# Performance work log

Hardware: AMD Instinct MI355X
Metric: run time of the kernel (lower is better)

The kernel has to match this reference:

```python
import jax, jax.numpy as jnp
from jax import lax
import numpy as np

SR = 44100
PI = 3.14159  # matches the constant used in the torch source
FREQ_HZ = 100.0
FREQ_RAD = 2.0 * PI * FREQ_HZ / SR
N_SAMPLES = 4_410_000  # 100 s of audio; exactly 10000 wavetable chunks of 441


def biquad_lowpass(x, f, q):
    # torchaudio.functional.lowpass_biquad, direct form II transposed
    w0 = 2.0 * jnp.pi * f / SR
    cosw = jnp.cos(w0)
    alpha = jnp.sin(w0) / (2.0 * q)
    b0 = (1.0 - cosw) / 2.0
    b1 = 1.0 - cosw
    b2 = (1.0 - cosw) / 2.0
    a0 = 1.0 + alpha
    a1 = -2.0 * cosw
    a2 = 1.0 - alpha
    b0, b1, b2, a1, a2 = b0 / a0, b1 / a0, b2 / a0, a1 / a0, a2 / a0

    def step(carry, xn):
        s1, s2 = carry
        y = b0 * xn + s1
        s1n = b1 * xn - a1 * y + s2
        s2n = b2 * xn - a2 * y
        return (s1n, s2n), y

    zero = jnp.zeros((), x.dtype)
    _, y = lax.scan(step, (zero, zero), x)
    return y


def setup_inputs() -> dict:
    key = jax.random.key(0)
    ks = jax.random.split(key, 6)
    wsz = int(SR // FREQ_HZ)  # 441
    return {
        "feedback_line": 0.1 * jax.random.normal(ks[0], (N_SAMPLES,), jnp.float32),
        "h": jax.random.uniform(ks[1], (1, 9), jnp.float32),
        "t": jnp.arange(N_SAMPLES, dtype=jnp.float32) / SR,
        "wavetable_noise": 2.0 * jax.random.uniform(ks[2], (wsz,), jnp.float32) - 1.0,
        "W1": 0.1 * jax.random.normal(ks[3], (9, 128), jnp.float32),
        "b1": jnp.zeros((128,), jnp.float32),
        "W2": 0.1 * jax.random.normal(ks[4], (128, 5), jnp.float32),
        "b2": jnp.array([0.5, 1.0, 0.5, 0.05, 1.0], jnp.float32),
        "lp_cutoff": jnp.float32(8000.0),  # LearnableLowpass(sr, 8000.0)
        "env_params": jnp.array([0.1, 1.0, 0.5], jnp.float32),  # LearnableASR(3): attack, sustain, release
        "fade": jnp.linspace(1.0, 0.0, 256, dtype=jnp.float32),
        "freq_rad": FREQ_RAD,  # static python float
        "output_length_samples": N_SAMPLES,  # static python int
    }


def reference(feedback_line, h, t, wavetable_noise, W1, b1, W2, b2, lp_cutoff, env_params, fade, freq_rad, output_length_samples):
    # hamps_to_decay MLP: Linear(9,128) -> ReLU -> Linear(128,5) -> ReLU
    latents = jax.nn.relu(jax.nn.relu(h @ W1 + b1) @ W2 + b2)  # [1, 5]
    decay = jnp.clip(latents[0, 0] / 10.0 + 0.9, 0.9, 0.999)

    freq = freq_rad * SR / (2.0 * PI)
    wsz = int(SR // freq)  # static wavetable size

    # wavetable = 2*rand-1, then biquad lowpass with learned cutoff/Q, then LearnableLowpass
    lowpass_freq = jnp.clip(latents[0, 1] * SR / 4.0, 100.0, SR / 2.0 - 1.0)
    lowpass_q = jnp.clip(latents[0, 2], 0.1, 0.999)
    wt = biquad_lowpass(wavetable_noise, lowpass_freq, lowpass_q)
    wt = biquad_lowpass(wt, lp_cutoff, jnp.float32(0.707))  # self.lowpass

    feedbackamt = latents[0, 3]
    wt = lax.stop_gradient(wt)  # original detaches the wavetable before the recurrence

    # Karplus-Strong recurrence over chunks: sequential scan (data-dependent across steps)
    n_chunks = output_length_samples // wsz
    fb = feedback_line[: n_chunks * wsz].reshape(n_chunks, wsz)

    def step(cur, fb_chunk):
        cur = cur + feedbackamt * fb_chunk
        cur = decay * 0.5 * (cur + jnp.roll(cur, 1))
        return cur, cur

    last, chunks = lax.scan(step, wt, fb)
    samples = chunks.reshape(-1)

    rem = output_length_samples % wsz
    if rem > 0:  # static python branch
        extra = decay * 0.5 * (last + jnp.roll(last, 1))
        samples = jnp.concatenate([samples, extra[:rem]])

    out = samples.at[-256:].multiply(fade)

    # LearnableASR envelope: attack ramp, sustain level, release ramp
    a = jnp.abs(env_params[0]) + 1e-3
    s = env_params[1]
    r = jnp.abs(env_params[2]) + 1e-3
    T = t[-1]
    env = jnp.clip(t / a, 0.0, 1.0) * jnp.clip((T - t) / r, 0.0, 1.0) * s

    return out * env * latents[0, 4]
```

## Files before the change

kernel.cpp:

```cpp
#include <hip/hip_runtime.h>
#include <utility>

#define N_SAMP   4410000
#define WSZ      441
#define NC       10000
#define NB       250
#define LB       40
#define HB       20
#define TILEF    (LB*WSZ)
#define RD       16
#define TWO_PI_F 6.28318530717958647692f
#define FADE_START (N_SAMP - 256)
#define INV_SR   (1.0f/44100.0f)
#define INV441   (1.0f/441.0f)

#define WS_WT   0
#define WS_SLOT(a) (448 + (a)*448)
#define WS_NEED ((size_t)(448 + (NB-1)*448) * sizeof(float))

static_assert(NB * LB == NC, "block decomposition");
static_assert(LB == 2*HB, "two flush phases");

template <class F, int... Is>
__device__ __forceinline__ void unroll_impl(F f, std::integer_sequence<int, Is...>) {
    (f(std::integral_constant<int, Is>{}), ...);
}
template <int N, class F>
__device__ __forceinline__ void unroll_for(F f) {
    unroll_impl(f, std::make_integer_sequence<int, N>{});
}

__device__ __forceinline__ float hwsin(float rev) { return __builtin_amdgcn_sinf(rev); }
__device__ __forceinline__ float hwcos(float rev) { return __builtin_amdgcn_cosf(rev); }

__device__ __forceinline__ void gl2lds16(const float* gsrc_lane, float* lds_base_uniform) {
    __builtin_amdgcn_global_load_lds(
        (const __attribute__((address_space(1))) void*)gsrc_lane,
        (__attribute__((address_space(3))) void*)lds_base_uniform,
        16, 0, 0);
}

__device__ __forceinline__ void stage_tile7(const float* __restrict__ g,
                                            float* __restrict__ l,
                                            int nfloats, int tid) {
    const int wave = tid >> 6, lane = tid & 63;
    const int nfull = nfloats >> 8;
    for (int c = wave; c < nfull; c += 7)
        gl2lds16(g + (c << 8) + lane*4, l + (c << 8));
    const int rem = nfloats & 255;
    if (rem && wave == 0 && lane*4 < rem) {
        const int base = nfull << 8;
        gl2lds16(g + base + lane*4, l + base);
    }
}

__device__ __forceinline__ void bq_coefs(float f, float q,
    float& b0, float& b1, float& b2, float& a1, float& a2)
{
    float w0 = TWO_PI_F * f / 44100.0f;
    float cw = cosf(w0), sw = sinf(w0);
    float al = sw / (2.0f * q);
    float a0 = 1.0f + al;
    b0 = ((1.0f - cw) * 0.5f) / a0;
    b1 = (1.0f - cw) / a0;
    b2 = ((1.0f - cw) * 0.5f) / a0;
    a1 = (-2.0f * cw) / a0;
    a2 = (1.0f - al) / a0;
}

__device__ __forceinline__ void run_biquads(const float* __restrict__ noise,
    float lpf, float lpq, float f2, float* dst)
{
    float c10,c11,c12,c13,c14, c20,c21,c22,c23,c24;
    bq_coefs(lpf, lpq, c10,c11,c12,c13,c14);
    bq_coefs(f2, 0.707f, c20,c21,c22,c23,c24);
    float s11=0.f,s12=0.f,s21=0.f,s22=0.f;
    for (int m = 0; m < WSZ; ++m) {
        float x  = noise[m];
        float y1 = c10*x + s11;
        s11 = c11*x - c13*y1 + s12;
        s12 = c12*x - c14*y1;
        float y2 = c20*y1 + s21;
        s21 = c21*y1 - c23*y2 + s22;
        s22 = c22*y1 - c24*y2;
        dst[m] = y2;
    }
}

__device__ __forceinline__ void mlp_latents(
    const float* __restrict__ h, const float* __restrict__ W1,
    const float* __restrict__ b1v, const float* __restrict__ W2,
    const float* __restrict__ b2v, int lane, float lat[5])
{
    float hc0 = b1v[lane], hc1 = b1v[lane + 64];
    #pragma unroll
    for (int i = 0; i < 9; ++i) {
        float hv = h[i];
        hc0 = fmaf(hv, W1[i*128 + lane], hc0);
        hc1 = fmaf(hv, W1[i*128 + lane + 64], hc1);
    }
    hc0 = fmaxf(hc0, 0.f); hc1 = fmaxf(hc1, 0.f);
    float part[5];
    #pragma unroll
    for (int m = 0; m < 5; ++m)
        part[m] = fmaf(hc0, W2[lane*5 + m], hc1 * W2[(lane+64)*5 + m]);
    #pragma unroll
    for (int off = 32; off > 0; off >>= 1) {
        #pragma unroll
        for (int m = 0; m < 5; ++m)
            part[m] += __shfl_xor(part[m], off);
    }
    #pragma unroll
    for (int m = 0; m < 5; ++m)
        lat[m] = fmaxf(part[m] + b2v[m], 0.f);
}

__device__ __forceinline__ void biquad_wave(const float xin[7], float yout[7],
    float f, float q, int l)
{
    float b0,b1,b2,a1,a2;
    bq_coefs(f, q, b0,b1,b2,a1,a2);
    const float t1c = b1 - a1*b0;
    const float t2c = b2 - a2*b0;
    float m00=1.f,m01=0.f,m10=0.f,m11=1.f;
    float cv0=0.f, cv1=0.f;
    #pragma unroll
    for (int k = 0; k < 7; ++k) {
        float x = xin[k];
        float n0 = -a1*cv0 + cv1 + t1c*x;
        float n1 = -a2*cv0 + t2c*x;
        cv0 = n0; cv1 = n1;
        float r00 = -a1*m00 + m10, r01 = -a1*m01 + m11;
        float r10 = -a2*m00,       r11 = -a2*m01;
        m00=r00; m01=r01; m10=r10; m11=r11;
    }
    #pragma unroll
    for (int d = 1; d < 64; d <<= 1) {
        int srcl = l - d; int s2 = srcl < 0 ? 0 : srcl;
        float pm00=__shfl(m00,s2), pm01=__shfl(m01,s2);
        float pm10=__shfl(m10,s2), pm11=__shfl(m11,s2);
        float pc0=__shfl(cv0,s2), pc1=__shfl(cv1,s2);
        if (srcl >= 0) {
            float nc0 = m00*pc0 + m01*pc1 + cv0;
            float nc1 = m10*pc0 + m11*pc1 + cv1;
            float n00 = m00*pm00 + m01*pm10;
            float n01 = m00*pm01 + m01*pm11;
            float n10 = m10*pm00 + m11*pm10;
            float n11 = m10*pm01 + m11*pm11;
            m00=n00; m01=n01; m10=n10; m11=n11; cv0=nc0; cv1=nc1;
        }
    }
    int esrc = (l == 0) ? 0 : l - 1;
    float e0 = __shfl(cv0, esrc);
    float e1 = __shfl(cv1, esrc);
    float s1  = (l == 0) ? 0.f : e0;
    float s2v = (l == 0) ? 0.f : e1;
    #pragma unroll
    for (int k = 0; k < 7; ++k) {
        float x = xin[k];
        float y = b0*x + s1;
        float ns1 = b1*x - a1*y + s2v;
        s2v = b2*x - a2*y;
        s1 = ns1;
        yout[k] = y;
    }
}

__device__ __forceinline__ void fft441_fwd(const float* v, float* Zr, float* Zi,
    const float* c441, const float* s441, float* ws_slot, int tid)
{
    if (tid < 441) {
        const int bq = tid / 21, c = tid - 21*bq;
        float yr = 0.f, yi = 0.f;
        int pm = 0;
        #pragma unroll
        for (int a = 0; a < 21; ++a) {
            float x = v[21*a + bq];
            float cc = c441[21*pm], ss = s441[21*pm];
            yr = fmaf(x,  cc, yr);
            yi = fmaf(-x, ss, yi);
            pm += c; if (pm >= 21) pm -= 21;
        }
        const int bc = bq * c;
        float cB = c441[bc], sB = s441[bc];
        Zr[c*21 + bq] = yr*cB + yi*sB;
        Zi[c*21 + bq] = yi*cB - yr*sB;
    }
    __syncthreads();
    if (tid < 441) {
        const int c = tid / 21, d = tid - 21*c;
        float xr = 0.f, xi = 0.f;
        int pm = 0;
        const float* zr = Zr + c*21;
        const float* zi = Zi + c*21;
        #pragma unroll
        for (int bq = 0; bq < 21; ++bq) {
            float cc = c441[21*pm], ss = s441[21*pm];
            float gr = zr[bq], gi = zi[bq];
            xr = fmaf(gr, cc, fmaf(gi,  ss, xr));
            xi = fmaf(gi, cc, fmaf(-gr, ss, xi));
            pm += d; if (pm >= 21) pm -= 21;
        }
        const int jm = c + 21*d;
        if (jm < 221) {
            ws_slot[jm]       = xr;
            ws_slot[224 + jm] = xi;
        }
    }
}

__device__ __forceinline__ void fft441_inv(const float* SrF, const float* SiF,
    float* Hr, float* Hi, const float* c441, const float* s441,
    float* e_lds, int tid)
{
    if (tid < 441) {
        const int bq = tid / 21, c = tid - 21*bq;
        float gr = 0.f, gi = 0.f;
        int pm = 0;
        #pragma unroll
        for (int a = 0; a < 21; ++a) {
            float sr = SrF[21*a + bq], si = SiF[21*a + bq];
            float cc = c441[21*pm], ss = s441[21*pm];
            gr = fmaf(sr, cc, fmaf(-si, ss, gr));
            gi = fmaf(sr, ss, fmaf( si, cc, gi));
            pm += c; if (pm >= 21) pm -= 21;
        }
        const int bc = bq * c;
        float cB = c441[bc], sB = s441[bc];
        Hr[c*21 + bq] = gr*cB - gi*sB;
        Hi[c*21 + bq] = gr*sB + gi*cB;
    }
    __syncthreads();
    if (tid < 441) {
        const int c = tid / 21, d = tid - 21*c;
        float acc = 0.f;
        int pm = 0;
        const float* hr = Hr + c*21;
        const float* hi = Hi + c*21;
        #pragma unroll
        for (int bq = 0; bq < 21; ++bq) {
            float cc = c441[21*pm], ss = s441[21*pm];
            acc = fmaf(hr[bq], cc, fmaf(-hi[bq], ss, acc));
            pm += d; if (pm >= 21) pm -= 21;
        }
        e_lds[c + 21*d] = acc * (1.0f/441.0f);
    }
}

__global__ __launch_bounds__(448, 1) void k_front(
    const float* __restrict__ fb, const float* __restrict__ h,
    const float* __restrict__ noise, const float* __restrict__ W1,
    const float* __restrict__ b1v, const float* __restrict__ W2,
    const float* __restrict__ b2v, const float* __restrict__ lpcut,
    float* __restrict__ ws)
{
    __shared__ __align__(16) float fbL[TILEF + 24];
    __shared__ __align__(16) float v_lds[448];
    __shared__ __align__(16) float Zr[441], Zi[441];
    __shared__ float c441[441], s441[441];
    const int b = blockIdx.x;
    const int tid = threadIdx.x;
    const bool w0 = tid < 64;
    const int j = tid;
    const bool act = w0 && (j < 63);
    const int i0 = b * LB;

    stage_tile7(fb + i0*WSZ, fbL, TILEF, tid);
    if (tid < 441) {
        float ph = (float)tid * INV441;
        c441[tid] = hwcos(ph);
        s441[tid] = hwsin(ph);
    }

    float lat[5];
    mlp_latents(h, W1, b1v, W2, b2v, tid & 63, lat);
    const float decay = fminf(fmaxf(lat[0]/10.0f + 0.9f, 0.9f), 0.999f);
    const float famt  = lat[3];
    const float d2 = 0.5f * decay;
    const int src = (j == 0) ? 62 : j - 1;

    float cur[7];
    #pragma unroll
    for (int k = 0; k < 7; ++k) cur[k] = 0.f;
    if (w0 && b == 0) {
        const float lpf = fminf(fmaxf(lat[1]*44100.0f/4.0f, 100.0f), 22049.0f);
        const float lpq = fminf(fmaxf(lat[2], 0.1f), 0.999f);
        const float f2  = lpcut[0];
        float xin[7], y1[7], y2[7];
        #pragma unroll
        for (int k = 0; k < 7; ++k) xin[k] = act ? noise[7*j + k] : 0.f;
        biquad_wave(xin, y1, lpf, lpq, j);
        biquad_wave(y1, y2, f2, 0.707f, j);
        #pragma unroll
        for (int k = 0; k < 7; ++k) {
            cur[k] = act ? y2[k] : 0.f;
            if (act) ws[WS_WT + 7*j + k] = y2[k];
        }
    }
    __syncthreads();

    if (w0) {
        unroll_for<LB>([&](auto I) {
            constexpr int i = decltype(I)::value;
            float x[7];
            #pragma unroll
            for (int k = 0; k < 7; ++k) {
                float fv = act ? fbL[i*WSZ + 7*j + k] : 0.f;
                x[k] = fmaf(famt, fv, cur[k]);
            }
            float x6p = __shfl(x[6], src);
            cur[0] = d2 * (x[0] + x6p);
            #pragma unroll
            for (int k = 1; k < 7; ++k)
                cur[k] = d2 * (x[k] + x[k-1]);
        });
        if (act) {
            #pragma unroll
            for (int k = 0; k < 7; ++k) v_lds[7*j + k] = cur[k];
        }
    }
    __syncthreads();

    fft441_fwd(v_lds, Zr, Zi, c441, s441, ws + WS_SLOT(b), tid);
}

__global__ __launch_bounds__(256, 1) void k_scan(
    const float* __restrict__ h, const float* __restrict__ W1,
    const float* __restrict__ b1v, const float* __restrict__ W2,
    const float* __restrict__ b2v, float* __restrict__ ws)
{
    const int tid = threadIdx.x;
    float lat[5];
    mlp_latents(h, W1, b1v, W2, b2v, tid & 63, lat);
    const float decay = fminf(fmaxf(lat[0]/10.0f + 0.9f, 0.9f), 0.999f);
    if (tid >= 221) return;
    const float s = hwsin((float)tid * INV441);
    const float c = hwcos((float)tid * INV441);
    float lr = 0.5f*decay*(1.0f + c);
    float li = -0.5f*decay*s;
    float pr = 1.0f, pi = 0.0f, br = lr, bi = li;
    int e = LB;
    while (e) {
        if (e & 1) { float t = pr*br - pi*bi; pi = pr*bi + pi*br; pr = t; }
        float t2 = br*br - bi*bi; bi = 2.0f*br*bi; br = t2;
        e >>= 1;
    }
    const int NV = NB - 1;
    float sr = 0.0f, si = 0.0f;
    float cr[RD], ci[RD];
    #pragma unroll
    for (int d = 0; d < RD; ++d) {
        int idx = (d < NV) ? d : NV-1;
        cr[d] = ws[WS_SLOT(idx) + tid];
        ci[d] = ws[WS_SLOT(idx) + 224 + tid];
    }
    for (int base = 0; base < NV; base += RD) {
        float nr[RD], ni[RD];
        #pragma unroll
        for (int d = 0; d < RD; ++d) {
            int idx = base + RD + d; if (idx >= NV) idx = NV-1;
            nr[d] = ws[WS_SLOT(idx) + tid];
            ni[d] = ws[WS_SLOT(idx) + 224 + tid];
        }
        #pragma unroll
        for (int d = 0; d < RD; ++d) {
            int bb = base + d;
            if (bb < NV) {
                float t1 = pr*sr - pi*si + cr[d];
                si = pr*si + pi*sr + ci[d];
                sr = t1;
                ws[WS_SLOT(bb) + tid]       = sr;
                ws[WS_SLOT(bb) + 224 + tid] = si;
            }
        }
        #pragma unroll
        for (int d = 0; d < RD; ++d) { cr[d] = nr[d]; ci[d] = ni[d]; }
    }
}

__global__ __launch_bounds__(448, 1) void k_back(
    const float* __restrict__ fb, const float* __restrict__ h,
    const float* __restrict__ W1, const float* __restrict__ b1v,
    const float* __restrict__ W2, const float* __restrict__ b2v,
    const float* __restrict__ t_in, const float* __restrict__ envp,
    const float* __restrict__ fade, float* __restrict__ out,
    const float* __restrict__ ws)
{
    __shared__ __align__(16) float fbL[TILEF + 24];
    __shared__ float out_lds[HB*441];
    __shared__ __align__(16) float SrF[441], SiF[441];
    __shared__ __align__(16) float Hr[441], Hi[441];
    __shared__ __align__(16) float e_lds[448];
    __shared__ float c441[441], s441[441];
    const int b = blockIdx.x;
    const int tid = threadIdx.x;
    const bool w0 = tid < 64;
    const int j = tid;
    const bool act = w0 && (j < 63);
    const int i0 = b * LB;

    if (tid < 441) {
        float ph = (float)tid * INV441;
        c441[tid] = hwcos(ph);
        s441[tid] = hwsin(ph);
    }

    float lat[5];
    mlp_latents(h, W1, b1v, W2, b2v, tid & 63, lat);
    const float decay = fminf(fmaxf(lat[0]/10.0f + 0.9f, 0.9f), 0.999f);
    const float famt  = lat[3];
    const float gain  = lat[4];
    const float d2 = 0.5f * decay;
    const int src = (j == 0) ? 62 : j - 1;

    stage_tile7(fb + i0*WSZ, fbL, TILEF, tid);

    if (b == 0) {
        for (int m = tid; m < 441; m += 448) e_lds[m] = ws[WS_WT + m];
        __syncthreads();
    } else {
        if (tid < 221) {
            SrF[tid] = ws[WS_SLOT(b-1) + tid];
            SiF[tid] = ws[WS_SLOT(b-1) + 224 + tid];
        }
        __syncthreads();
        if (tid >= 221 && tid < 441) {
            SrF[tid] =  SrF[441 - tid];
            SiF[tid] = -SiF[441 - tid];
        }
        __syncthreads();
        fft441_inv(SrF, SiF, Hr, Hi, c441, s441, e_lds, tid);
        __syncthreads();
    }

    const float a_  = fabsf(envp[0]) + 1e-3f;
    const float sus = envp[1];
    const float rr  = fabsf(envp[2]) + 1e-3f;
    const float inv_a = 1.0f / a_;
    const float inv_r = 1.0f / rr;
    const float sg = sus * gain;
    const float T = t_in[N_SAMP - 1];

    float cur[7];
    #pragma unroll
    for (int k = 0; k < 7; ++k)
        cur[k] = act ? e_lds[7*j + k] : 0.f;

    auto compute_half = [&](auto PH) {
        constexpr int ph = decltype(PH)::value;
        if (w0) {
            unroll_for<HB>([&](auto I) {
                constexpr int il = decltype(I)::value;
                constexpr int i = ph*HB + il;
                float x[7];
                #pragma unroll
                for (int k = 0; k < 7; ++k) {
                    float fv = act ? fbL[i*WSZ + 7*j + k] : 0.f;
                    x[k] = fmaf(famt, fv, cur[k]);
                }
                float x6p = __shfl(x[6], src);
                cur[0] = d2 * (x[0] + x6p);
                #pragma unroll
                for (int k = 1; k < 7; ++k)
                    cur[k] = d2 * (x[k] + x[k-1]);
                if (act) {
                    #pragma unroll
                    for (int k = 0; k < 7; ++k)
                        out_lds[il*WSZ + 7*j + k] = cur[k];
                }
            });
        }
    };
    auto flush = [&](int ph) {
        const int s0 = (i0 + ph*HB) * WSZ;
        const float t_lo = (float)s0 * INV_SR;
        const float t_hi = (float)(s0 + HB*WSZ - 1) * INV_SR;
        const bool fastenv = (t_lo * inv_a >= 1.0f) &&
                             ((T - t_hi) * inv_r >= 1.0f) &&
                             (s0 + HB*WSZ <= FADE_START);
        if (fastenv) {
            for (int e = tid; e < HB*WSZ; e += 448)
                out[s0 + e] = out_lds[e] * sg;
        } else {
            for (int e = tid; e < HB*WSZ; e += 448) {
                const int idx = s0 + e;
                float tt = (float)idx * INV_SR;
                float ca  = fminf(tt * inv_a, 1.0f);
                float crr = fminf(fmaxf((T - tt) * inv_r, 0.0f), 1.0f);
                float val = out_lds[e] * (ca * crr * sg);
                if (idx >= FADE_START) val *= fade[idx - FADE_START];
                out[idx] = val;
            }
        }
    };

    compute_half(std::integral_constant<int,0>{});
    __syncthreads();
    flush(0);
    __syncthreads();
    compute_half(std::integral_constant<int,1>{});
    __syncthreads();
    flush(1);
}

__global__ __launch_bounds__(448) void k_naive(
    const float* __restrict__ fb, const float* __restrict__ h,
    const float* __restrict__ t_in, const float* __restrict__ noise,
    const float* __restrict__ W1, const float* __restrict__ b1v,
    const float* __restrict__ W2, const float* __restrict__ b2v,
    const float* __restrict__ lpcut, const float* __restrict__ envp,
    const float* __restrict__ fade, float* __restrict__ out)
{
    __shared__ float hid[128];
    __shared__ float lat[5];
    __shared__ float wt[WSZ];
    __shared__ float buf[2][448];
    const int j = threadIdx.x;
    if (j < 128) {
        float acc = b1v[j];
        #pragma unroll
        for (int i = 0; i < 9; ++i) acc = acc + h[i] * W1[i*128 + j];
        hid[j] = fmaxf(acc, 0.0f);
    }
    __syncthreads();
    if (j < 5) {
        float a = b2v[j];
        for (int k = 0; k < 128; ++k) a = a + hid[k] * W2[k*5 + j];
        lat[j] = fmaxf(a, 0.0f);
    }
    __syncthreads();
    if (j == 0) {
        float lpf = fminf(fmaxf(lat[1]*44100.0f/4.0f, 100.0f), 22049.0f);
        float lpq = fminf(fmaxf(lat[2], 0.1f), 0.999f);
        run_biquads(noise, lpf, lpq, lpcut[0], wt);
    }
    __syncthreads();
    const float decay = fminf(fmaxf(lat[0]/10.0f + 0.9f, 0.9f), 0.999f);
    const float famt = lat[3];
    const float gain = lat[4];
    const float d2 = 0.5f * decay;
    const float a_  = fabsf(envp[0]) + 1e-3f;
    const float sus = envp[1];
    const float rr  = fabsf(envp[2]) + 1e-3f;
    const float inv_a = 1.0f / a_, inv_r = 1.0f / rr;
    const float T = t_in[N_SAMP - 1];
    const bool act = j < WSZ;
    const int jm1 = (j == 0) ? (WSZ - 1) : (j - 1);
    float cur = act ? wt[j] : 0.0f;
    for (int i = 0; i < NC; ++i) {
        float x = cur + famt * (act ? fb[i*WSZ + j] : 0.0f);
        buf[i&1][j] = x;
        __syncthreads();
        cur = d2 * (x + buf[i&1][jm1]);
        const int idx = i*WSZ + j;
        float val = cur;
        if (idx >= FADE_START) val *= fade[idx - FADE_START];
        float tt = act ? t_in[idx] : 0.0f;
        float ca  = fminf(fmaxf(tt * inv_a, 0.0f), 1.0f);
        float cr2 = fminf(fmaxf((T - tt) * inv_r, 0.0f), 1.0f);
        val = val * (ca * cr2 * sus) * gain;
        if (act) out[idx] = val;
    }
}

extern "C" void kernel_launch(void* const* d_in, const int* in_sizes, int n_in,
                              void* d_out, int out_size, void* d_ws, size_t ws_size,
                              hipStream_t stream) {
    const float* fb   = (const float*)d_in[0];
    const float* h    = (const float*)d_in[1];
    const float* t    = (const float*)d_in[2];
    const float* nz   = (const float*)d_in[3];
    const float* W1   = (const float*)d_in[4];
    const float* b1v  = (const float*)d_in[5];
    const float* W2   = (const float*)d_in[6];
    const float* b2v  = (const float*)d_in[7];
    const float* lpc  = (const float*)d_in[8];
    const float* envp = (const float*)d_in[9];
    const float* fade = (const float*)d_in[10];
    float* out = (float*)d_out;
    float* ws  = (float*)d_ws;

    if (ws_size < WS_NEED) {
        k_naive<<<1, 448, 0, stream>>>(fb, h, t, nz, W1, b1v, W2, b2v, lpc, envp, fade, out);
        return;
    }
    k_front<<<NB-1, 448, 0, stream>>>(fb, h, nz, W1, b1v, W2, b2v, lpc, ws);
    k_scan <<<1,    256, 0, stream>>>(h, W1, b1v, W2, b2v, ws);
    k_back <<<NB,   448, 0, stream>>>(fb, h, W1, b1v, W2, b2v, t, envp, fade, out, ws);
}
```

Baseline: 54.17 us.

## Fold sequential block-prefix scan into k_back, each block recomputing its own prefix

Removes the single-block k_scan kernel. Each k_back block now computes its own inclusive prefix over the preceding block-summary spectra, reading from the workspace. This drops a kernel launch and a serial dependency stage at the cost of redundant work: later blocks iterate over up to 249 slots, so the last block does as much serial work as the old scan. The fb tile staging is also moved earlier so its loads can overlap the prefix computation.

```diff
diff --git a/kernel.cpp b/kernel.cpp
--- a/kernel.cpp
+++ b/kernel.cpp
@@ -324,60 +324,6 @@
     fft441_fwd(v_lds, Zr, Zi, c441, s441, ws + WS_SLOT(b), tid);
 }
 
-__global__ __launch_bounds__(256, 1) void k_scan(
-    const float* __restrict__ h, const float* __restrict__ W1,
-    const float* __restrict__ b1v, const float* __restrict__ W2,
-    const float* __restrict__ b2v, float* __restrict__ ws)
-{
-    const int tid = threadIdx.x;
-    float lat[5];
-    mlp_latents(h, W1, b1v, W2, b2v, tid & 63, lat);
-    const float decay = fminf(fmaxf(lat[0]/10.0f + 0.9f, 0.9f), 0.999f);
-    if (tid >= 221) return;
-    const float s = hwsin((float)tid * INV441);
-    const float c = hwcos((float)tid * INV441);
-    float lr = 0.5f*decay*(1.0f + c);
-    float li = -0.5f*decay*s;
-    float pr = 1.0f, pi = 0.0f, br = lr, bi = li;
-    int e = LB;
-    while (e) {
-        if (e & 1) { float t = pr*br - pi*bi; pi = pr*bi + pi*br; pr = t; }
-        float t2 = br*br - bi*bi; bi = 2.0f*br*bi; br = t2;
-        e >>= 1;
-    }
-    const int NV = NB - 1;
-    float sr = 0.0f, si = 0.0f;
-    float cr[RD], ci[RD];
-    #pragma unroll
-    for (int d = 0; d < RD; ++d) {
-        int idx = (d < NV) ? d : NV-1;
-        cr[d] = ws[WS_SLOT(idx) + tid];
-        ci[d] = ws[WS_SLOT(idx) + 224 + tid];
-    }
-    for (int base = 0; base < NV; base += RD) {
-        float nr[RD], ni[RD];
-        #pragma unroll
-        for (int d = 0; d < RD; ++d) {
-            int idx = base + RD + d; if (idx >= NV) idx = NV-1;
-            nr[d] = ws[WS_SLOT(idx) + tid];
-            ni[d] = ws[WS_SLOT(idx) + 224 + tid];
-        }
-        #pragma unroll
-        for (int d = 0; d < RD; ++d) {
-            int bb = base + d;
-            if (bb < NV) {
-                float t1 = pr*sr - pi*si + cr[d];
-                si = pr*si + pi*sr + ci[d];
-                sr = t1;
-                ws[WS_SLOT(bb) + tid]       = sr;
-                ws[WS_SLOT(bb) + 224 + tid] = si;
-            }
-        }
-        #pragma unroll
-        for (int d = 0; d < RD; ++d) { cr[d] = nr[d]; ci[d] = ni[d]; }
-    }
-}
-
 __global__ __launch_bounds__(448, 1) void k_back(
     const float* __restrict__ fb, const float* __restrict__ h,
     const float* __restrict__ W1, const float* __restrict__ b1v,
@@ -399,6 +345,7 @@
     const bool act = w0 && (j < 63);
     const int i0 = b * LB;
 
+    stage_tile7(fb + i0*WSZ, fbL, TILEF, tid);
     if (tid < 441) {
         float ph = (float)tid * INV441;
         c441[tid] = hwcos(ph);
@@ -413,15 +360,51 @@
     const float d2 = 0.5f * decay;
     const int src = (j == 0) ? 62 : j - 1;
 
-    stage_tile7(fb + i0*WSZ, fbL, TILEF, tid);
-
     if (b == 0) {
         for (int m = tid; m < 441; m += 448) e_lds[m] = ws[WS_WT + m];
         __syncthreads();
     } else {
         if (tid < 221) {
-            SrF[tid] = ws[WS_SLOT(b-1) + tid];
-            SiF[tid] = ws[WS_SLOT(b-1) + 224 + tid];
+            const float s = hwsin((float)tid * INV441);
+            const float c = hwcos((float)tid * INV441);
+            float lr = 0.5f*decay*(1.0f + c);
+            float li = -0.5f*decay*s;
+            float pr = 1.0f, pi = 0.0f, br = lr, bi = li;
+            int e = LB;
+            while (e) {
+                if (e & 1) { float t = pr*br - pi*bi; pi = pr*bi + pi*br; pr = t; }
+                float t2 = br*br - bi*bi; bi = 2.0f*br*bi; br = t2;
+                e >>= 1;
+            }
+            const int n = b;
+            float sr = 0.f, si = 0.f;
+            float cr[RD], ci[RD];
+            #pragma unroll
+            for (int d = 0; d < RD; ++d) {
+                int idx = (d < n) ? d : n-1;
+                cr[d] = ws[WS_SLOT(idx) + tid];
+                ci[d] = ws[WS_SLOT(idx) + 224 + tid];
+            }
+            for (int base = 0; base < n; base += RD) {
+                float nr[RD], ni[RD];
+                #pragma unroll
+                for (int d = 0; d < RD; ++d) {
+                    int idx = base + RD + d; if (idx >= n) idx = n-1;
+                    nr[d] = ws[WS_SLOT(idx) + tid];
+                    ni[d] = ws[WS_SLOT(idx) + 224 + tid];
+                }
+                #pragma unroll
+                for (int d = 0; d < RD; ++d) {
+                    if (base + d < n) {
+                        float t1 = fmaf(pr, sr, fmaf(-pi, si, cr[d]));
+                        si = fmaf(pr, si, fmaf(pi, sr, ci[d]));
+                        sr = t1;
+                    }
+                }
+                #pragma unroll
+                for (int d = 0; d < RD; ++d) { cr[d] = nr[d]; ci[d] = ni[d]; }
+            }
+            SrF[tid] = sr; SiF[tid] = si;
         }
         __syncthreads();
         if (tid >= 221 && tid < 441) {
@@ -585,6 +568,5 @@
         return;
     }
     k_front<<<NB-1, 448, 0, stream>>>(fb, h, nz, W1, b1v, W2, b2v, lpc, ws);
-    k_scan <<<1,    256, 0, stream>>>(h, W1, b1v, W2, b2v, ws);
     k_back <<<NB,   448, 0, stream>>>(fb, h, W1, b1v, W2, b2v, t, envp, fade, out, ws);
 }
```

Result: faster. 45.23 us, median of 2 (-16.5%).
